# Kernel optimization log

Measured on AMD Instinct MI355X. Metric: run time of the kernel, lower is better.

## Reference

```python
import jax, jax.numpy as jnp
import numpy as np

B, T, C = 4, 2048, 1024
N_HEAD = 16
HEAD_DIM = C // N_HEAD


def setup_inputs() -> dict:
    key = jax.random.key(0)
    k1, k2, k3 = jax.random.split(key, 3)
    scale = 0.02
    x = jax.random.normal(k1, (B, T, C), dtype=jnp.float32)
    W_attn = jax.random.normal(k2, (C, 3 * C), dtype=jnp.float32) * scale
    b_attn = jnp.zeros((3 * C,), dtype=jnp.float32)
    W_proj = jax.random.normal(k3, (C, C), dtype=jnp.float32) * scale
    b_proj = jnp.zeros((C,), dtype=jnp.float32)
    return {"x": x, "W_attn": W_attn, "b_attn": b_attn, "W_proj": W_proj, "b_proj": b_proj}


def reference(x, W_attn, b_attn, W_proj, b_proj):
    Bx, Tx, Cx = x.shape
    qkv = x @ W_attn + b_attn                      # [B,T,3C]
    q, k, v = jnp.split(qkv, 3, axis=-1)
    def split_heads(t):
        return t.reshape(Bx, Tx, N_HEAD, HEAD_DIM).transpose(0, 2, 1, 3)  # [B,H,T,D]
    q, k, v = split_heads(q), split_heads(k), split_heads(v)
    att = jnp.einsum('bhqd,bhkd->bhqk', q, k) / jnp.sqrt(jnp.float32(HEAD_DIM))
    causal = jnp.tril(jnp.ones((Tx, Tx), dtype=bool))
    att = jnp.where(causal, att, jnp.float32(-jnp.inf))
    att = jax.nn.softmax(att, axis=-1)
    y = jnp.einsum('bhqk,bhkd->bhqd', att, v)      # [B,H,T,D]
    y = y.transpose(0, 2, 1, 3).reshape(Bx, Tx, Cx)
    return y @ W_proj + b_proj
```

## Files before the change

kernel.cpp:

```cpp
#include <hip/hip_runtime.h>
#include <hip/hip_bf16.h>
#include <math.h>

#define B_  4
#define T_  2048
#define C_  1024
#define NH  16
#define HD  64
#define M_  (B_ * T_)
#define N_QKV (3 * C_)
#define KDIM 1024
#define SCALE2 0.18033688011112042f

typedef __attribute__((ext_vector_type(8))) short short8;
typedef __attribute__((ext_vector_type(4))) short bs4;
typedef __attribute__((ext_vector_type(4))) float f32x4;
typedef __attribute__((ext_vector_type(16))) float f32x16;
typedef __attribute__((ext_vector_type(4))) unsigned u32x4;

__device__ __forceinline__ short f2bs(float f) {
  __hip_bfloat16 h = __float2bfloat16(f);
  return *reinterpret_cast<short*>(&h);
}
__device__ __forceinline__ unsigned packrn(float a, float b) {
  __hip_bfloat162 h = __float22bfloat162_rn(float2{a, b});
  unsigned u;
  __builtin_memcpy(&u, &h, 4);
  return u;
}

__device__ __forceinline__ void gload16(const void* g, void* l) {
  __builtin_amdgcn_global_load_lds(
      (const __attribute__((address_space(1))) void*)g,
      (__attribute__((address_space(3))) void*)l, 16, 0, 0);
}

__device__ __forceinline__ void wtrans_body(
    const float* __restrict__ W, short* __restrict__ Wt, int Ncols, int qcols,
    int bid2, int tid, short (*t)[33])
{
  const int nb = Ncols / 32;
  const int bn = bid2 % nb, bk = bid2 / nb;
  const int r = tid >> 3, c4 = (tid & 7) * 4;
  const float cs = (bn * 32 < qcols) ? SCALE2 : 1.f;
  f32x4 v = *reinterpret_cast<const f32x4*>(
      W + (size_t)(bk * 32 + r) * Ncols + bn * 32 + c4);
  #pragma unroll
  for (int j = 0; j < 4; ++j) t[r][c4 + j] = f2bs(v[j] * cs);
  __syncthreads();
  bs4 o;
  #pragma unroll
  for (int j = 0; j < 4; ++j) o[j] = t[c4 + j][r];
  *reinterpret_cast<bs4*>(Wt + (size_t)(bn * 32 + r) * KDIM + bk * 32 + c4) = o;
}

__global__ __launch_bounds__(256) void prep_kernel(
    const float* __restrict__ x,  short* __restrict__ xb,
    const float* __restrict__ Wa, short* __restrict__ WaT,
    const float* __restrict__ Wp, short* __restrict__ WpT)
{
  __shared__ short t[32][33];
  const int bid = blockIdx.x;
  const int tid = threadIdx.x;
  if (bid < 4096) {
    const int i = (bid * 256 + tid) * 8;
    f32x4 a = *reinterpret_cast<const f32x4*>(x + i);
    f32x4 b = *reinterpret_cast<const f32x4*>(x + i + 4);
    short8 o;
    #pragma unroll
    for (int j = 0; j < 4; ++j) { o[j] = f2bs(a[j]); o[4 + j] = f2bs(b[j]); }
    *reinterpret_cast<short8*>(xb + i) = o;
  } else if (bid < 7168) {
    wtrans_body(Wa, WaT, N_QKV, C_, bid - 4096, tid, t);
  } else {
    wtrans_body(Wp, WpT, C_, 0, bid - 7168, tid, t);
  }
}

template<bool OUT_BF16>
__global__ __launch_bounds__(256) void gemm128b_kernel(
    const short* __restrict__ A, const short* __restrict__ Bt,
    const float* __restrict__ bias, void* __restrict__ outptr, int N, int nq)
{
  __shared__ short As[128 * 64];
  __shared__ short Bs[128 * 64];

  const int tid  = threadIdx.x;
  const int lane = tid & 63;
  const int w    = tid >> 6;
  const int wr   = w >> 1, wc = w & 1;
  const int rl   = lane & 15, kg = lane >> 4;
  const int nblk = N >> 7;
  const int m0 = (blockIdx.x / nblk) << 7;
  const int n0 = (blockIdx.x % nblk) << 7;

  f32x4 acc[4][4] = {};

  const int srow = w * 8 + (lane >> 3);
  const int scol = ((lane & 7) ^ ((lane >> 3) & 7)) * 8;
  const short* pa = A  + (size_t)(m0 + srow) * KDIM + scol;
  const short* pb = Bt + (size_t)(n0 + srow) * KDIM + scol;

  for (int k0 = 0; k0 < KDIM; k0 += 64) {
    __syncthreads();
    #pragma unroll
    for (int i = 0; i < 4; ++i) {
      gload16(pa + (size_t)i * 32 * KDIM + k0, &As[i * 2048 + w * 512]);
      gload16(pb + (size_t)i * 32 * KDIM + k0, &Bs[i * 2048 + w * 512]);
    }
    __syncthreads();

    #pragma unroll
    for (int kk = 0; kk < 2; ++kk) {
      const int sl = ((kk * 4 + kg) ^ (rl & 7)) * 8;
      short8 af[4], bf[4];
      #pragma unroll
      for (int i = 0; i < 4; ++i) {
        af[i] = *reinterpret_cast<short8*>(&As[(wr * 64 + i * 16 + rl) * 64 + sl]);
        bf[i] = *reinterpret_cast<short8*>(&Bs[(wc * 64 + i * 16 + rl) * 64 + sl]);
      }
      #pragma unroll
      for (int mi = 0; mi < 4; ++mi)
        #pragma unroll
        for (int ni = 0; ni < 4; ++ni)
          acc[mi][ni] = __builtin_amdgcn_mfma_f32_16x16x32_bf16(
              af[mi], bf[ni], acc[mi][ni], 0, 0, 0);
    }
  }

  #pragma unroll
  for (int ni = 0; ni < 4; ++ni) {
    const int col = n0 + wc * 64 + ni * 16 + rl;
    float bv = bias[col];
    if (col < nq) bv *= SCALE2;
    #pragma unroll
    for (int mi = 0; mi < 4; ++mi) {
      #pragma unroll
      for (int r = 0; r < 4; ++r) {
        const int row = m0 + wr * 64 + mi * 16 + kg * 4 + r;
        const float v = acc[mi][ni][r] + bv;
        if constexpr (OUT_BF16)
          ((short*)outptr)[(size_t)row * N + col] = f2bs(v);
        else
          ((float*)outptr)[(size_t)row * N + col] = v;
      }
    }
  }
}

__global__ __launch_bounds__(256) void attn_mfma13_kernel(
    const short* __restrict__ qkv, short* __restrict__ y)
{
  __shared__ short Ks[2][64 * 64];
  __shared__ short Vt[2][64 * 64];

  const int tid  = threadIdx.x;
  const int lane = tid & 63;
  const int w    = tid >> 6;
  const int q32  = lane & 31;
  const int hi   = lane >> 5;

  const int bid  = blockIdx.x;
  const int qi   = 15 - (bid >> 6);
  const int bh   = bid & 63;
  const int b    = bh >> 4, h = bh & 15;
  const size_t bT = (size_t)b * T_;

  const int kr0 = tid >> 3;
  const int kl0 = (tid & 7) ^ ((tid >> 3) & 7);
  const int kr1 = (tid + 256) >> 3;
  const int kl1 = (tid & 7) ^ (((tid + 256) >> 3) & 7);
  const size_t kbase0 = (bT + kr0) * N_QKV + C_ + h * HD + kl0 * 8;
  const size_t kbase1 = (bT + kr1) * N_QKV + C_ + h * HD + kl1 * 8;
  short* const kdst0 = &Ks[0][(w * 64) * 8];
  short* const kdst1 = &Ks[0][(w * 64 + 256) * 8];

  const int kp = tid & 31;
  const int d0 = (tid >> 5) * 8;
  const size_t vbaseA = (bT + 2 * kp) * N_QKV + 2 * C_ + h * HD + d0;
  const size_t vbaseB = vbaseA + N_QKV;
  const int vws = ((kp >> 2) << 3) + ((kp & 3) << 1);

  const int ksl = q32 & 7;

  const int nkb = 2 * qi + 2;
  const int wq0 = qi * 128 + w * 32;
  const int q   = wq0 + q32;

  short8 qf[4];
  #pragma unroll
  for (int kd = 0; kd < 4; ++kd)
    qf[kd] = *reinterpret_cast<const short8*>(
        qkv + (bT + q) * N_QKV + h * HD + kd * 16 + hi * 8);

  f32x16 o0 = {}, o1 = {};
  float m_ = -INFINITY, l_ = 0.f;

  {
    gload16(qkv + kbase0, kdst0);
    gload16(qkv + kbase1, kdst1);
    short8 va = *reinterpret_cast<const short8*>(qkv + vbaseA);
    short8 vb = *reinterpret_cast<const short8*>(qkv + vbaseB);
    #pragma unroll
    for (int j = 0; j < 8; ++j) {
      unsigned pw = (unsigned)(unsigned short)va[j] |
                    ((unsigned)(unsigned short)vb[j] << 16);
      *reinterpret_cast<unsigned*>(
          &Vt[0][(d0 + j) * 64 + (vws ^ (j << 3))]) = pw;
    }
  }
  __syncthreads();

  int cur = 0;
  for (int kb = 0; kb < nkb; ++kb) {
    const bool more = (kb + 1 < nkb);
    short8 va, vb;
    if (more) {
      const size_t koff = (size_t)(kb + 1) * 64 * N_QKV;
      gload16(qkv + kbase0 + koff, kdst0 + (cur ^ 1) * 4096);
      gload16(qkv + kbase1 + koff, kdst1 + (cur ^ 1) * 4096);
      va = *reinterpret_cast<const short8*>(qkv + vbaseA + koff);
      vb = *reinterpret_cast<const short8*>(qkv + vbaseB + koff);
    }

    const int kmin = kb * 64;
    if (kmin <= wq0 + 31) {
      const short* ksc = &Ks[cur][0];
      const short* vtc = &Vt[cur][0];

      f32x16 s0 = {}, s1 = {};
      #pragma unroll
      for (int kd = 0; kd < 4; ++kd) {
        const int sl = ((2 * kd + hi) ^ ksl) * 8;
        short8 kf0 = *reinterpret_cast<const short8*>(&ksc[q32 * 64 + sl]);
        short8 kf1 = *reinterpret_cast<const short8*>(&ksc[(32 + q32) * 64 + sl]);
        s0 = __builtin_amdgcn_mfma_f32_32x32x16_bf16(kf0, qf[kd], s0, 0, 0, 0);
        s1 = __builtin_amdgcn_mfma_f32_32x32x16_bf16(kf1, qf[kd], s1, 0, 0, 0);
      }

      if (kmin + 63 > wq0) {
        const int qrel = q - kmin - 4 * hi;
        #pragma unroll
        for (int e = 0; e < 16; ++e) {
          const int ko = (e & 3) + 8 * (e >> 2);
          if (ko > qrel)      s0[e] = -INFINITY;
          if (ko + 32 > qrel) s1[e] = -INFINITY;
        }
      }

      float mv[16];
      #pragma unroll
      for (int e = 0; e < 16; ++e) mv[e] = fmaxf(s0[e], s1[e]);
      #pragma unroll
      for (int st = 8; st >= 1; st >>= 1)
        #pragma unroll
        for (int e = 0; e < st; ++e) mv[e] = fmaxf(mv[e], mv[e + st]);
      float mx = fmaxf(mv[0], __shfl_xor(mv[0], 32, 64));

      if (!__all(mx <= m_ + 8.f)) {
        const float mn = fmaxf(m_, mx);
        const float cr = exp2f(m_ - mn);
        m_ = mn;
        l_ *= cr;
        #pragma unroll
        for (int e = 0; e < 16; ++e) { o0[e] *= cr; o1[e] *= cr; }
      }

      #pragma unroll
      for (int e = 0; e < 16; ++e) {
        s0[e] = exp2f(s0[e] - m_);
        s1[e] = exp2f(s1[e] - m_);
      }
      float sv[16];
      #pragma unroll
      for (int e = 0; e < 16; ++e) sv[e] = s0[e] + s1[e];
      #pragma unroll
      for (int st = 8; st >= 1; st >>= 1)
        #pragma unroll
        for (int e = 0; e < st; ++e) sv[e] += sv[e + st];
      l_ += sv[0] + __shfl_xor(sv[0], 32, 64);

      unsigned pk[2][4][2], sw[2][4][2];
      #pragma unroll
      for (int gg = 0; gg < 4; ++gg)
        #pragma unroll
        for (int p = 0; p < 2; ++p) {
          pk[0][gg][p] = packrn(s0[4 * gg + 2 * p], s0[4 * gg + 2 * p + 1]);
          pk[1][gg][p] = packrn(s1[4 * gg + 2 * p], s1[4 * gg + 2 * p + 1]);
          sw[0][gg][p] = (unsigned)__shfl_xor((int)pk[0][gg][p], 32, 64);
          sw[1][gg][p] = (unsigned)__shfl_xor((int)pk[1][gg][p], 32, 64);
        }

      #pragma unroll
      for (int kk = 0; kk < 4; ++kk) {
        const int c = kk >> 1, a2 = 2 * (kk & 1);
        u32x4 t;
        t[0] = hi ? sw[c][a2 + 1][0] : pk[c][a2][0];
        t[1] = hi ? sw[c][a2 + 1][1] : pk[c][a2][1];
        t[2] = hi ? pk[c][a2 + 1][0] : sw[c][a2][0];
        t[3] = hi ? pk[c][a2 + 1][1] : sw[c][a2][1];
        const short8 pb = __builtin_bit_cast(short8, t);
        const int sl = ((2 * kk + hi) ^ ksl) * 8;
        short8 vf0 = *reinterpret_cast<const short8*>(&vtc[q32 * 64 + sl]);
        short8 vf1 = *reinterpret_cast<const short8*>(&vtc[(32 + q32) * 64 + sl]);
        o0 = __builtin_amdgcn_mfma_f32_32x32x16_bf16(vf0, pb, o0, 0, 0, 0);
        o1 = __builtin_amdgcn_mfma_f32_32x32x16_bf16(vf1, pb, o1, 0, 0, 0);
      }
    }

    if (more) {
      #pragma unroll
      for (int j = 0; j < 8; ++j) {
        unsigned pw = (unsigned)(unsigned short)va[j] |
                      ((unsigned)(unsigned short)vb[j] << 16);
        *reinterpret_cast<unsigned*>(
            &Vt[cur ^ 1][(d0 + j) * 64 + (vws ^ (j << 3))]) = pw;
      }
    }
    __syncthreads();
    cur ^= 1;
  }

  const float inv = 1.f / l_;
  short* const yp = y + (bT + q) * C_ + h * HD;
  #pragma unroll
  for (int gg = 0; gg < 4; ++gg) {
    bs4 ov0, ov1;
    #pragma unroll
    for (int t = 0; t < 4; ++t) {
      ov0[t] = f2bs(o0[4 * gg + t] * inv);
      ov1[t] = f2bs(o1[4 * gg + t] * inv);
    }
    *reinterpret_cast<bs4*>(yp + 8 * gg + 4 * hi)      = ov0;
    *reinterpret_cast<bs4*>(yp + 32 + 8 * gg + 4 * hi) = ov1;
  }
}

extern "C" void kernel_launch(void* const* d_in, const int* in_sizes, int n_in,
                              void* d_out, int out_size, void* d_ws, size_t ws_size,
                              hipStream_t stream) {
  const float* x  = (const float*)d_in[0];
  const float* Wa = (const float*)d_in[1];
  const float* ba = (const float*)d_in[2];
  const float* Wp = (const float*)d_in[3];
  const float* bp = (const float*)d_in[4];

  short* qkvb = (short*)d_ws;
  short* xb   = qkvb + (size_t)M_ * N_QKV;
  short* yb   = xb;
  short* WaT  = xb + (size_t)M_ * C_;
  short* WpT  = WaT + (size_t)N_QKV * KDIM;

  prep_kernel<<<8192, 256, 0, stream>>>(x, xb, Wa, WaT, Wp, WpT);
  gemm128b_kernel<true><<<(M_ / 128) * (N_QKV / 128), 256, 0, stream>>>(
      xb, WaT, ba, qkvb, N_QKV, C_);
  attn_mfma13_kernel<<<16 * B_ * NH, 256, 0, stream>>>(qkvb, yb);
  gemm128b_kernel<false><<<(M_ / 128) * (C_ / 128), 256, 0, stream>>>(
      yb, WpT, bp, d_out, C_, 0);
}
```

Before: 195.7 us.

## Pair complementary causal query tiles in one 512-thread attention block

Each attention block now has 8 waves split into two groups of four. One group handles query tile 15-gb and the other handles tile gb, so every block does a balanced amount of causal work and the grid halves to 512 blocks. The two groups share the same K/V tiles in LDS, with the loading work now spread over 512 threads (one 16-byte K load and 4-element V pieces per thread). The short-tile group sits idle for the later iterations but still has to pass every barrier, and the larger blocks may lower occupancy.

```diff
diff --git a/kernel.cpp b/kernel.cpp
--- a/kernel.cpp
+++ b/kernel.cpp
@@ -148,7 +148,7 @@
   }
 }
 
-__global__ __launch_bounds__(256) void attn_mfma13_kernel(
+__global__ __launch_bounds__(512) void attn_mfma14_kernel(
     const short* __restrict__ qkv, short* __restrict__ y)
 {
   __shared__ short Ks[2][64 * 64];
@@ -156,35 +156,35 @@
 
   const int tid  = threadIdx.x;
   const int lane = tid & 63;
-  const int w    = tid >> 6;
+  const int w4   = (tid >> 6) & 3;
+  const int wgrp = tid >> 8;
   const int q32  = lane & 31;
   const int hi   = lane >> 5;
 
   const int bid  = blockIdx.x;
-  const int qi   = 15 - (bid >> 6);
+  const int gb   = bid >> 6;
   const int bh   = bid & 63;
   const int b    = bh >> 4, h = bh & 15;
   const size_t bT = (size_t)b * T_;
 
-  const int kr0 = tid >> 3;
-  const int kl0 = (tid & 7) ^ ((tid >> 3) & 7);
-  const int kr1 = (tid + 256) >> 3;
-  const int kl1 = (tid & 7) ^ (((tid + 256) >> 3) & 7);
-  const size_t kbase0 = (bT + kr0) * N_QKV + C_ + h * HD + kl0 * 8;
-  const size_t kbase1 = (bT + kr1) * N_QKV + C_ + h * HD + kl1 * 8;
-  short* const kdst0 = &Ks[0][(w * 64) * 8];
-  short* const kdst1 = &Ks[0][(w * 64 + 256) * 8];
+  const int qi   = wgrp ? gb : (15 - gb);
+  const int nkb  = 2 * (15 - gb) + 2;
+
+  const int krow = tid >> 3;
+  const int klog = (tid & 7) ^ (krow & 7);
+  const size_t kbase = (bT + krow) * N_QKV + C_ + h * HD + klog * 8;
+  short* const kdst = &Ks[0][tid * 8];
 
   const int kp = tid & 31;
-  const int d0 = (tid >> 5) * 8;
+  const int d0 = (tid >> 5) * 4;
+  const int ph = ((tid >> 5) & 1) * 4;
   const size_t vbaseA = (bT + 2 * kp) * N_QKV + 2 * C_ + h * HD + d0;
   const size_t vbaseB = vbaseA + N_QKV;
   const int vws = ((kp >> 2) << 3) + ((kp & 3) << 1);
 
   const int ksl = q32 & 7;
 
-  const int nkb = 2 * qi + 2;
-  const int wq0 = qi * 128 + w * 32;
+  const int wq0 = qi * 128 + w4 * 32;
   const int q   = wq0 + q32;
 
   short8 qf[4];
@@ -197,16 +197,15 @@
   float m_ = -INFINITY, l_ = 0.f;
 
   {
-    gload16(qkv + kbase0, kdst0);
-    gload16(qkv + kbase1, kdst1);
-    short8 va = *reinterpret_cast<const short8*>(qkv + vbaseA);
-    short8 vb = *reinterpret_cast<const short8*>(qkv + vbaseB);
-    #pragma unroll
-    for (int j = 0; j < 8; ++j) {
+    gload16(qkv + kbase, kdst);
+    bs4 va = *reinterpret_cast<const bs4*>(qkv + vbaseA);
+    bs4 vb = *reinterpret_cast<const bs4*>(qkv + vbaseB);
+    #pragma unroll
+    for (int j = 0; j < 4; ++j) {
       unsigned pw = (unsigned)(unsigned short)va[j] |
                     ((unsigned)(unsigned short)vb[j] << 16);
       *reinterpret_cast<unsigned*>(
-          &Vt[0][(d0 + j) * 64 + (vws ^ (j << 3))]) = pw;
+          &Vt[0][(d0 + j) * 64 + (vws ^ ((ph + j) << 3))]) = pw;
     }
   }
   __syncthreads();
@@ -214,13 +213,12 @@
   int cur = 0;
   for (int kb = 0; kb < nkb; ++kb) {
     const bool more = (kb + 1 < nkb);
-    short8 va, vb;
+    bs4 va, vb;
     if (more) {
       const size_t koff = (size_t)(kb + 1) * 64 * N_QKV;
-      gload16(qkv + kbase0 + koff, kdst0 + (cur ^ 1) * 4096);
-      gload16(qkv + kbase1 + koff, kdst1 + (cur ^ 1) * 4096);
-      va = *reinterpret_cast<const short8*>(qkv + vbaseA + koff);
-      vb = *reinterpret_cast<const short8*>(qkv + vbaseB + koff);
+      gload16(qkv + kbase + koff, kdst + (cur ^ 1) * 4096);
+      va = *reinterpret_cast<const bs4*>(qkv + vbaseA + koff);
+      vb = *reinterpret_cast<const bs4*>(qkv + vbaseB + koff);
     }
 
     const int kmin = kb * 64;
@@ -310,11 +308,11 @@
 
     if (more) {
       #pragma unroll
-      for (int j = 0; j < 8; ++j) {
+      for (int j = 0; j < 4; ++j) {
         unsigned pw = (unsigned)(unsigned short)va[j] |
                       ((unsigned)(unsigned short)vb[j] << 16);
         *reinterpret_cast<unsigned*>(
-            &Vt[cur ^ 1][(d0 + j) * 64 + (vws ^ (j << 3))]) = pw;
+            &Vt[cur ^ 1][(d0 + j) * 64 + (vws ^ ((ph + j) << 3))]) = pw;
       }
     }
     __syncthreads();
@@ -354,7 +352,7 @@
   prep_kernel<<<8192, 256, 0, stream>>>(x, xb, Wa, WaT, Wp, WpT);
   gemm128b_kernel<true><<<(M_ / 128) * (N_QKV / 128), 256, 0, stream>>>(
       xb, WaT, ba, qkvb, N_QKV, C_);
-  attn_mfma13_kernel<<<16 * B_ * NH, 256, 0, stream>>>(qkvb, yb);
+  attn_mfma14_kernel<<<512, 512, 0, stream>>>(qkvb, yb);
   gemm128b_kernel<false><<<(M_ / 128) * (C_ / 128), 256, 0, stream>>>(
       yb, WpT, bp, d_out, C_, 0);
 }
```

Measured after the change: 214.5 us. 1.1x slower.
